# Performance work log

Measured on AMD Instinct MI355X. Metric: run time of the kernel, lower is better.

## Reference

```python
import jax, jax.numpy as jnp
import numpy as np

WINDOW = 15  # window_size from init


def setup_inputs() -> dict:
    key = jax.random.key(0)
    ks = jax.random.split(key, 8)
    B, S, H, G = 16, 4096, 768, 16
    sequence_output = jax.random.normal(ks[0], (B, S, H), dtype=jnp.float32)
    pooled_output = jax.random.normal(ks[1], (B, H), dtype=jnp.float32)
    token_type_ids = jnp.zeros((B, S), dtype=jnp.int64)
    word_mask = jax.random.randint(ks[2], (B, S), 0, 2, dtype=jnp.int64)
    gap_ids = jax.random.randint(ks[3], (B, G), 0, S, dtype=jnp.int64)
    gap_W = 0.02 * jax.random.normal(ks[4], (3 * H,), dtype=jnp.float32)
    gap_b = jnp.zeros((), dtype=jnp.float32)
    cls_W = 0.02 * jax.random.normal(ks[5], (3 * H,), dtype=jnp.float32)
    cls_b = jnp.zeros((), dtype=jnp.float32)
    return {"sequence_output": sequence_output, "pooled_output": pooled_output,
            "token_type_ids": token_type_ids, "word_mask": word_mask,
            "gap_ids": gap_ids, "gap_W": gap_W, "gap_b": gap_b,
            "cls_W": cls_W, "cls_b": cls_b}


def reference(sequence_output, pooled_output, token_type_ids, word_mask,
              gap_ids, gap_W, gap_b, cls_W, cls_b):
    B, S, H = sequence_output.shape
    G = gap_ids.shape[1]
    w = WINDOW
    Wlen = 2 * w + 1

    # gap token embeddings: [B, G, H]
    gaps = jnp.take_along_axis(sequence_output, gap_ids[:, :, None], axis=1)

    base_mask = (token_type_ids == 0) & (word_mask != 0)  # [B, S]

    # Sliding window gather around each gap (equivalent to the original
    # full-sequence masked reduction, since masked entries are exactly 0).
    offsets = jnp.arange(-w, w + 1)  # [Wlen]
    raw_idx = gap_ids[:, :, None] + offsets  # [B, G, Wlen]
    valid = (raw_idx >= 0) & (raw_idx < S)
    idx = jnp.clip(raw_idx, 0, S - 1)
    flat = idx.reshape(B, G * Wlen)
    win_mask = valid & jnp.take_along_axis(base_mask, flat, axis=1).reshape(B, G, Wlen)
    win_vals = jnp.take_along_axis(sequence_output, flat[:, :, None], axis=1).reshape(B, G, Wlen, H)

    # original does max(window * mask): masked positions contribute 0,
    # and the sequence always has positions outside the window -> max with 0
    masked_max = jnp.where(win_mask[..., None], win_vals, -jnp.inf).max(axis=2)
    window_max_pool = jnp.maximum(masked_max, 0.0)  # [B, G, H]
    num_tokens = win_mask.sum(axis=2).astype(jnp.float32)[:, :, None]
    window_avg_pool = jnp.einsum('bgw,bgwh->bgh', win_mask.astype(jnp.float32), win_vals) / num_tokens

    # full-text pooling
    text_masked_max = jnp.where(base_mask[:, :, None], sequence_output, -jnp.inf).max(axis=1)
    text_max_pool = jnp.maximum(text_masked_max, 0.0)  # [B, H]
    text_num = base_mask.sum(axis=1).astype(jnp.float32)[:, None]
    text_avg_pool = jnp.einsum('bs,bsh->bh', base_mask.astype(jnp.float32), sequence_output) / text_num

    gap_features = jnp.concatenate([gaps, window_max_pool, window_avg_pool], axis=-1)  # [B, G, 3H]
    cls_features = jnp.concatenate([pooled_output, text_max_pool, text_avg_pool], axis=-1)  # [B, 3H]

    gap_scores = gap_features @ gap_W + gap_b  # [B, G]
    cls_scores = (cls_features @ cls_W + cls_b)[:, None]  # [B, 1]
    return jnp.concatenate([cls_scores, gap_scores], axis=1)  # [B, 1+G]
```

## Files before the change

kernel.cpp:

```cpp
#include <hip/hip_runtime.h>
#include <math.h>

#define NB 16
#define NS 4096
#define NH 768
#define NG 16
#define WRAD 15
#define WLEN 31
#define NH4 192
#define OUTW (1 + NG)
#define NCH 32
#define CHUNK 128

__device__ inline float4 f4max(float4 a, float4 b) {
    return make_float4(fmaxf(a.x, b.x), fmaxf(a.y, b.y), fmaxf(a.z, b.z), fmaxf(a.w, b.w));
}
__device__ inline float4 f4add(float4 a, float4 b) {
    return make_float4(a.x + b.x, a.y + b.y, a.z + b.z, a.w + b.w);
}
__device__ inline float f4dot(float4 a, float4 b) {
    return a.x * b.x + a.y * b.y + a.z * b.z + a.w * b.w;
}

__device__ inline float block_reduce_192(float v, float* sbuf) {
    int tid = threadIdx.x;
    sbuf[tid] = v;
    if (tid < 64) sbuf[192 + tid] = 0.0f;
    __syncthreads();
    for (int off = 128; off > 0; off >>= 1) {
        if (tid < off) sbuf[tid] += sbuf[tid + off];
        __syncthreads();
    }
    float r = sbuf[0];
    __syncthreads();
    return r;
}

__global__ __launch_bounds__(192) void fused_kernel(
    const float* __restrict__ seq, const int* __restrict__ tt,
    const int* __restrict__ wm, const int* __restrict__ gids,
    const float* __restrict__ gapW, const float* __restrict__ gapb,
    float* __restrict__ pmax, float* __restrict__ psum,
    int* __restrict__ pcnt, float* __restrict__ out) {
    const int blk = blockIdx.x;
    const int tid = threadIdx.x;

    __shared__ float sbuf[256];
    __shared__ int s_idx[CHUNK];
    __shared__ unsigned long long s_wmask[2];
    __shared__ int s_misc[2];

    const float4 ninf4 = make_float4(-INFINITY, -INFINITY, -INFINITY, -INFINITY);
    const float4 zero4 = make_float4(0.f, 0.f, 0.f, 0.f);

    if (blk < NB * NCH) {
        const int b = blk / NCH;
        const int ss = blk % NCH;
        const int s0 = ss * CHUNK;

        if (tid < CHUNK) {
            const int s = s0 + tid;
            bool v = (tt[b * NS + s] == 0) && (wm[b * NS + s] != 0);
            unsigned long long m = __ballot(v);
            if ((tid & 63) == 0) s_wmask[tid >> 6] = m;
        }
        __syncthreads();
        if (tid < CHUNK) {
            const int w = tid >> 6, l = tid & 63;
            const unsigned long long m = s_wmask[w];
            if ((m >> l) & 1ull) {
                int pos = (w ? __popcll(s_wmask[0]) : 0) +
                          __popcll(m & ((1ull << l) - 1ull));
                s_idx[pos] = s0 + tid;
            }
        }
        if (tid == 0)
            s_misc[0] = __popcll(s_wmask[0]) + __popcll(s_wmask[1]);
        __syncthreads();
        const int n = s_misc[0];

        const float4* rowbase = (const float4*)(seq + (size_t)b * NS * NH);
        float4 mx = ninf4;
        float4 sm = zero4;
        int i = 0;
        for (; i + 4 <= n; i += 4) {
            const int i0 = s_idx[i], i1 = s_idx[i + 1], i2 = s_idx[i + 2], i3 = s_idx[i + 3];
            float4 v0 = rowbase[(size_t)i0 * NH4 + tid];
            float4 v1 = rowbase[(size_t)i1 * NH4 + tid];
            float4 v2 = rowbase[(size_t)i2 * NH4 + tid];
            float4 v3 = rowbase[(size_t)i3 * NH4 + tid];
            mx = f4max(mx, f4max(f4max(v0, v1), f4max(v2, v3)));
            sm = f4add(sm, f4add(f4add(v0, v1), f4add(v2, v3)));
        }
        for (; i < n; ++i) {
            float4 v = rowbase[(size_t)s_idx[i] * NH4 + tid];
            mx = f4max(mx, v);
            sm = f4add(sm, v);
        }
        const size_t o = ((size_t)(b * NCH + ss)) * NH4 + tid;
        ((float4*)pmax)[o] = mx;
        ((float4*)psum)[o] = sm;
        if (tid == 0) pcnt[b * NCH + ss] = n;
    } else {
        const int bg = blk - NB * NCH;
        const int b = bg >> 4;
        const int g = bg & 15;

        if (tid == 0) s_misc[1] = gids[b * NG + g];
        __syncthreads();
        const int gi = s_misc[1];

        if (tid < 64) {
            bool v = false;
            if (tid < WLEN) {
                const int idx = gi - WRAD + tid;
                v = (idx >= 0) && (idx < NS) && (tt[b * NS + idx] == 0) &&
                    (wm[b * NS + idx] != 0);
            }
            unsigned long long m = __ballot(v);
            if (tid == 0) s_wmask[0] = m;
        }
        __syncthreads();
        const unsigned long long vm = s_wmask[0];
        const float count = (float)__popcll(vm);

        const float4* rowbase = (const float4*)(seq + (size_t)b * NS * NH);
        const float4 gv = rowbase[(size_t)gi * NH4 + tid];

        float4 mx = ninf4;
        float4 sm = zero4;
#pragma unroll 4
        for (int j = 0; j < WLEN; ++j) {
            int idx = gi - WRAD + j;
            idx = idx < 0 ? 0 : (idx > NS - 1 ? NS - 1 : idx);
            const float4 v = rowbase[(size_t)idx * NH4 + tid];
            const bool val = (vm >> j) & 1ull;
            mx.x = val ? fmaxf(mx.x, v.x) : mx.x;
            mx.y = val ? fmaxf(mx.y, v.y) : mx.y;
            mx.z = val ? fmaxf(mx.z, v.z) : mx.z;
            mx.w = val ? fmaxf(mx.w, v.w) : mx.w;
            sm.x += val ? v.x : 0.f;
            sm.y += val ? v.y : 0.f;
            sm.z += val ? v.z : 0.f;
            sm.w += val ? v.w : 0.f;
        }
        const float4 wmax = f4max(mx, zero4);
        const float4 wavg = make_float4(sm.x / count, sm.y / count,
                                        sm.z / count, sm.w / count);

        const float4* w0 = (const float4*)gapW;
        const float4* w1 = (const float4*)(gapW + NH);
        const float4* w2 = (const float4*)(gapW + 2 * NH);
        float part = f4dot(gv, w0[tid]) + f4dot(wmax, w1[tid]) + f4dot(wavg, w2[tid]);
        float total = block_reduce_192(part, sbuf);
        if (tid == 0) out[b * OUTW + 1 + g] = total + gapb[0];
    }
}

__global__ __launch_bounds__(192) void cls_kernel(
    const float* __restrict__ pooled, const float* __restrict__ pmax,
    const float* __restrict__ psum, const int* __restrict__ pcnt,
    const float* __restrict__ clsW, const float* __restrict__ clsb,
    float* __restrict__ out) {
    const int b = blockIdx.x;
    const int tid = threadIdx.x;
    __shared__ float sbuf[256];

    float c = (tid < NCH) ? (float)pcnt[b * NCH + tid] : 0.f;
    const float count = block_reduce_192(c, sbuf);

    const float4* pm4 = (const float4*)pmax;
    const float4* ps4 = (const float4*)psum;
    float4 mx = make_float4(-INFINITY, -INFINITY, -INFINITY, -INFINITY);
    float4 sm = make_float4(0.f, 0.f, 0.f, 0.f);
#pragma unroll 8
    for (int ch = 0; ch < NCH; ++ch) {
        const size_t o = ((size_t)(b * NCH + ch)) * NH4 + tid;
        mx = f4max(mx, pm4[o]);
        sm = f4add(sm, ps4[o]);
    }
    const float4 zero4 = make_float4(0.f, 0.f, 0.f, 0.f);
    const float4 tmax = f4max(mx, zero4);
    const float4 tavg = make_float4(sm.x / count, sm.y / count,
                                    sm.z / count, sm.w / count);

    const float4* p4 = (const float4*)(pooled + (size_t)b * NH);
    const float4* w0 = (const float4*)clsW;
    const float4* w1 = (const float4*)(clsW + NH);
    const float4* w2 = (const float4*)(clsW + 2 * NH);
    float part = f4dot(p4[tid], w0[tid]) + f4dot(tmax, w1[tid]) + f4dot(tavg, w2[tid]);
    float total = block_reduce_192(part, sbuf);
    if (tid == 0) out[b * OUTW + 0] = total + clsb[0];
}

extern "C" void kernel_launch(void* const* d_in, const int* in_sizes, int n_in,
                              void* d_out, int out_size, void* d_ws, size_t ws_size,
                              hipStream_t stream) {
    const float* seq    = (const float*)d_in[0];
    const float* pooled = (const float*)d_in[1];
    const int*   tt     = (const int*)d_in[2];
    const int*   wm     = (const int*)d_in[3];
    const int*   gids   = (const int*)d_in[4];
    const float* gapW   = (const float*)d_in[5];
    const float* gapb   = (const float*)d_in[6];
    const float* clsW   = (const float*)d_in[7];
    const float* clsb   = (const float*)d_in[8];
    float* out = (float*)d_out;

    float* pmax = (float*)d_ws;
    float* psum = pmax + (size_t)NB * NCH * NH;
    int*   pcnt = (int*)(psum + (size_t)NB * NCH * NH);

    fused_kernel<<<NB * NCH + NB * NG, 192, 0, stream>>>(
        seq, tt, wm, gids, gapW, gapb, pmax, psum, pcnt, out);
    cls_kernel<<<NB, 192, 0, stream>>>(pooled, pmax, psum, pcnt, clsW, clsb, out);
}
```

Before: 286.7 us.

## Fuse cls reduction into main kernel via last-block atomic arrival counter

Removes the separate cls_kernel launch. The last chunk block to finish for each batch, detected with an atomic arrival counter, now does the final cross-chunk max/sum reduction and the cls dot product, while a second atomic accumulates token counts. Gap blocks are moved to the front of the grid, and the chunk gather loop is unrolled to 8 rows for more loads in flight. In exchange it adds a hipMemsetAsync per call, threadfences and atomics, and a serialized tail on the last-arriving block.

New measurement: 364.1 us. 1.27x slower.

```diff
diff --git a/kernel.cpp b/kernel.cpp
--- a/kernel.cpp
+++ b/kernel.cpp
@@ -37,78 +37,35 @@
 }
 
 __global__ __launch_bounds__(192) void fused_kernel(
-    const float* __restrict__ seq, const int* __restrict__ tt,
-    const int* __restrict__ wm, const int* __restrict__ gids,
+    const float* __restrict__ seq, const float* __restrict__ pooled,
+    const int* __restrict__ tt, const int* __restrict__ wm,
+    const int* __restrict__ gids,
     const float* __restrict__ gapW, const float* __restrict__ gapb,
+    const float* __restrict__ clsW, const float* __restrict__ clsb,
     float* __restrict__ pmax, float* __restrict__ psum,
-    int* __restrict__ pcnt, float* __restrict__ out) {
+    unsigned int* __restrict__ arrive, unsigned int* __restrict__ tokcnt,
+    float* __restrict__ out) {
     const int blk = blockIdx.x;
     const int tid = threadIdx.x;
 
     __shared__ float sbuf[256];
     __shared__ int s_idx[CHUNK];
     __shared__ unsigned long long s_wmask[2];
-    __shared__ int s_misc[2];
+    __shared__ int s_n;
+    __shared__ int s_gid;
+    __shared__ int s_last;
+    __shared__ unsigned int s_tok;
 
     const float4 ninf4 = make_float4(-INFINITY, -INFINITY, -INFINITY, -INFINITY);
     const float4 zero4 = make_float4(0.f, 0.f, 0.f, 0.f);
 
-    if (blk < NB * NCH) {
-        const int b = blk / NCH;
-        const int ss = blk % NCH;
-        const int s0 = ss * CHUNK;
-
-        if (tid < CHUNK) {
-            const int s = s0 + tid;
-            bool v = (tt[b * NS + s] == 0) && (wm[b * NS + s] != 0);
-            unsigned long long m = __ballot(v);
-            if ((tid & 63) == 0) s_wmask[tid >> 6] = m;
-        }
-        __syncthreads();
-        if (tid < CHUNK) {
-            const int w = tid >> 6, l = tid & 63;
-            const unsigned long long m = s_wmask[w];
-            if ((m >> l) & 1ull) {
-                int pos = (w ? __popcll(s_wmask[0]) : 0) +
-                          __popcll(m & ((1ull << l) - 1ull));
-                s_idx[pos] = s0 + tid;
-            }
-        }
-        if (tid == 0)
-            s_misc[0] = __popcll(s_wmask[0]) + __popcll(s_wmask[1]);
-        __syncthreads();
-        const int n = s_misc[0];
-
-        const float4* rowbase = (const float4*)(seq + (size_t)b * NS * NH);
-        float4 mx = ninf4;
-        float4 sm = zero4;
-        int i = 0;
-        for (; i + 4 <= n; i += 4) {
-            const int i0 = s_idx[i], i1 = s_idx[i + 1], i2 = s_idx[i + 2], i3 = s_idx[i + 3];
-            float4 v0 = rowbase[(size_t)i0 * NH4 + tid];
-            float4 v1 = rowbase[(size_t)i1 * NH4 + tid];
-            float4 v2 = rowbase[(size_t)i2 * NH4 + tid];
-            float4 v3 = rowbase[(size_t)i3 * NH4 + tid];
-            mx = f4max(mx, f4max(f4max(v0, v1), f4max(v2, v3)));
-            sm = f4add(sm, f4add(f4add(v0, v1), f4add(v2, v3)));
-        }
-        for (; i < n; ++i) {
-            float4 v = rowbase[(size_t)s_idx[i] * NH4 + tid];
-            mx = f4max(mx, v);
-            sm = f4add(sm, v);
-        }
-        const size_t o = ((size_t)(b * NCH + ss)) * NH4 + tid;
-        ((float4*)pmax)[o] = mx;
-        ((float4*)psum)[o] = sm;
-        if (tid == 0) pcnt[b * NCH + ss] = n;
-    } else {
-        const int bg = blk - NB * NCH;
-        const int b = bg >> 4;
-        const int g = bg & 15;
-
-        if (tid == 0) s_misc[1] = gids[b * NG + g];
-        __syncthreads();
-        const int gi = s_misc[1];
+    if (blk < NB * NG) {
+        const int b = blk >> 4;
+        const int g = blk & 15;
+
+        if (tid == 0) s_gid = gids[b * NG + g];
+        __syncthreads();
+        const int gi = s_gid;
 
         if (tid < 64) {
             bool v = false;
@@ -154,43 +111,104 @@
         float part = f4dot(gv, w0[tid]) + f4dot(wmax, w1[tid]) + f4dot(wavg, w2[tid]);
         float total = block_reduce_192(part, sbuf);
         if (tid == 0) out[b * OUTW + 1 + g] = total + gapb[0];
+    } else {
+        const int t = blk - NB * NG;
+        const int b = t / NCH;
+        const int ss = t % NCH;
+        const int s0 = ss * CHUNK;
+
+        if (tid < CHUNK) {
+            const int s = s0 + tid;
+            bool v = (tt[b * NS + s] == 0) && (wm[b * NS + s] != 0);
+            unsigned long long m = __ballot(v);
+            if ((tid & 63) == 0) s_wmask[tid >> 6] = m;
+        }
+        __syncthreads();
+        if (tid < CHUNK) {
+            const int w = tid >> 6, l = tid & 63;
+            const unsigned long long m = s_wmask[w];
+            if ((m >> l) & 1ull) {
+                int pos = (w ? __popcll(s_wmask[0]) : 0) +
+                          __popcll(m & ((1ull << l) - 1ull));
+                s_idx[pos] = s0 + tid;
+            }
+        }
+        if (tid == 0)
+            s_n = __popcll(s_wmask[0]) + __popcll(s_wmask[1]);
+        __syncthreads();
+        const int n = s_n;
+
+        const float4* rowbase = (const float4*)(seq + (size_t)b * NS * NH);
+        float4 mx = ninf4;
+        float4 sm = zero4;
+        int i = 0;
+        for (; i + 8 <= n; i += 8) {
+            float4 v0 = rowbase[(size_t)s_idx[i] * NH4 + tid];
+            float4 v1 = rowbase[(size_t)s_idx[i + 1] * NH4 + tid];
+            float4 v2 = rowbase[(size_t)s_idx[i + 2] * NH4 + tid];
+            float4 v3 = rowbase[(size_t)s_idx[i + 3] * NH4 + tid];
+            float4 v4 = rowbase[(size_t)s_idx[i + 4] * NH4 + tid];
+            float4 v5 = rowbase[(size_t)s_idx[i + 5] * NH4 + tid];
+            float4 v6 = rowbase[(size_t)s_idx[i + 6] * NH4 + tid];
+            float4 v7 = rowbase[(size_t)s_idx[i + 7] * NH4 + tid];
+            mx = f4max(mx, f4max(f4max(f4max(v0, v1), f4max(v2, v3)),
+                                 f4max(f4max(v4, v5), f4max(v6, v7))));
+            sm = f4add(sm, f4add(f4add(f4add(v0, v1), f4add(v2, v3)),
+                                 f4add(f4add(v4, v5), f4add(v6, v7))));
+        }
+        for (; i + 4 <= n; i += 4) {
+            float4 v0 = rowbase[(size_t)s_idx[i] * NH4 + tid];
+            float4 v1 = rowbase[(size_t)s_idx[i + 1] * NH4 + tid];
+            float4 v2 = rowbase[(size_t)s_idx[i + 2] * NH4 + tid];
+            float4 v3 = rowbase[(size_t)s_idx[i + 3] * NH4 + tid];
+            mx = f4max(mx, f4max(f4max(v0, v1), f4max(v2, v3)));
+            sm = f4add(sm, f4add(f4add(v0, v1), f4add(v2, v3)));
+        }
+        for (; i < n; ++i) {
+            float4 v = rowbase[(size_t)s_idx[i] * NH4 + tid];
+            mx = f4max(mx, v);
+            sm = f4add(sm, v);
+        }
+        const size_t o = ((size_t)(b * NCH + ss)) * NH4 + tid;
+        ((float4*)pmax)[o] = mx;
+        ((float4*)psum)[o] = sm;
+
+        __threadfence();
+        __syncthreads();
+        if (tid == 0) {
+            atomicAdd(&tokcnt[b], (unsigned int)n);
+            __threadfence();
+            unsigned int old = atomicAdd(&arrive[b], 1u);
+            s_last = (old == NCH - 1);
+            if (s_last) s_tok = atomicAdd(&tokcnt[b], 0u);
+        }
+        __syncthreads();
+        if (s_last) {
+            __threadfence();
+            const float count = (float)s_tok;
+            const float4* pm4 = (const float4*)pmax;
+            const float4* ps4 = (const float4*)psum;
+            float4 cmx = ninf4;
+            float4 csm = zero4;
+#pragma unroll 8
+            for (int ch = 0; ch < NCH; ++ch) {
+                const size_t co = ((size_t)(b * NCH + ch)) * NH4 + tid;
+                cmx = f4max(cmx, pm4[co]);
+                csm = f4add(csm, ps4[co]);
+            }
+            const float4 tmax = f4max(cmx, zero4);
+            const float4 tavg = make_float4(csm.x / count, csm.y / count,
+                                            csm.z / count, csm.w / count);
+            const float4* p4 = (const float4*)(pooled + (size_t)b * NH);
+            const float4* w0 = (const float4*)clsW;
+            const float4* w1 = (const float4*)(clsW + NH);
+            const float4* w2 = (const float4*)(clsW + 2 * NH);
+            float part = f4dot(p4[tid], w0[tid]) + f4dot(tmax, w1[tid]) +
+                         f4dot(tavg, w2[tid]);
+            float total = block_reduce_192(part, sbuf);
+            if (tid == 0) out[b * OUTW + 0] = total + clsb[0];
+        }
     }
-}
-
-__global__ __launch_bounds__(192) void cls_kernel(
-    const float* __restrict__ pooled, const float* __restrict__ pmax,
-    const float* __restrict__ psum, const int* __restrict__ pcnt,
-    const float* __restrict__ clsW, const float* __restrict__ clsb,
-    float* __restrict__ out) {
-    const int b = blockIdx.x;
-    const int tid = threadIdx.x;
-    __shared__ float sbuf[256];
-
-    float c = (tid < NCH) ? (float)pcnt[b * NCH + tid] : 0.f;
-    const float count = block_reduce_192(c, sbuf);
-
-    const float4* pm4 = (const float4*)pmax;
-    const float4* ps4 = (const float4*)psum;
-    float4 mx = make_float4(-INFINITY, -INFINITY, -INFINITY, -INFINITY);
-    float4 sm = make_float4(0.f, 0.f, 0.f, 0.f);
-#pragma unroll 8
-    for (int ch = 0; ch < NCH; ++ch) {
-        const size_t o = ((size_t)(b * NCH + ch)) * NH4 + tid;
-        mx = f4max(mx, pm4[o]);
-        sm = f4add(sm, ps4[o]);
-    }
-    const float4 zero4 = make_float4(0.f, 0.f, 0.f, 0.f);
-    const float4 tmax = f4max(mx, zero4);
-    const float4 tavg = make_float4(sm.x / count, sm.y / count,
-                                    sm.z / count, sm.w / count);
-
-    const float4* p4 = (const float4*)(pooled + (size_t)b * NH);
-    const float4* w0 = (const float4*)clsW;
-    const float4* w1 = (const float4*)(clsW + NH);
-    const float4* w2 = (const float4*)(clsW + 2 * NH);
-    float part = f4dot(p4[tid], w0[tid]) + f4dot(tmax, w1[tid]) + f4dot(tavg, w2[tid]);
-    float total = block_reduce_192(part, sbuf);
-    if (tid == 0) out[b * OUTW + 0] = total + clsb[0];
 }
 
 extern "C" void kernel_launch(void* const* d_in, const int* in_sizes, int n_in,
@@ -209,9 +227,12 @@
 
     float* pmax = (float*)d_ws;
     float* psum = pmax + (size_t)NB * NCH * NH;
-    int*   pcnt = (int*)(psum + (size_t)NB * NCH * NH);
-
-    fused_kernel<<<NB * NCH + NB * NG, 192, 0, stream>>>(
-        seq, tt, wm, gids, gapW, gapb, pmax, psum, pcnt, out);
-    cls_kernel<<<NB, 192, 0, stream>>>(pooled, pmax, psum, pcnt, clsW, clsb, out);
-}
+    unsigned int* arrive = (unsigned int*)(psum + (size_t)NB * NCH * NH);
+    unsigned int* tokcnt = arrive + NB;
+
+    hipMemsetAsync(arrive, 0, 2 * NB * sizeof(unsigned int), stream);
+
+    fused_kernel<<<NB * NG + NB * NCH, 192, 0, stream>>>(
+        seq, pooled, tt, wm, gids, gapW, gapb, clsW, clsb,
+        pmax, psum, arrive, tokcnt, out);
+}
```

## Stream all rows with predicated masking instead of compacted index gather

Applied to the files above, without the earlier changes.

Text pooling blocks now read every row in a 64-row chunk contiguously with 8-way unrolled loads and apply the word mask via predication, instead of compacting masked indices in shared memory and gathering only those rows. Chunks are halved to double block count, and gap-window blocks are scheduled first in the grid. This removes the index-compaction sync and dependent index loads and gives regular, deep memory-level parallelism, at the cost of reading masked-out rows (about twice the bytes for half-dense masks).

After: 318.1 us. 11.0% more time.

```diff
diff --git a/kernel.cpp b/kernel.cpp
--- a/kernel.cpp
+++ b/kernel.cpp
@@ -9,8 +9,8 @@
 #define WLEN 31
 #define NH4 192
 #define OUTW (1 + NG)
-#define NCH 32
-#define CHUNK 128
+#define NCH 64
+#define CHUNK 64
 
 __device__ inline float4 f4max(float4 a, float4 b) {
     return make_float4(fmaxf(a.x, b.x), fmaxf(a.y, b.y), fmaxf(a.z, b.z), fmaxf(a.w, b.w));
@@ -46,69 +46,19 @@
     const int tid = threadIdx.x;
 
     __shared__ float sbuf[256];
-    __shared__ int s_idx[CHUNK];
-    __shared__ unsigned long long s_wmask[2];
-    __shared__ int s_misc[2];
+    __shared__ unsigned long long s_mask;
+    __shared__ int s_gid;
 
     const float4 ninf4 = make_float4(-INFINITY, -INFINITY, -INFINITY, -INFINITY);
     const float4 zero4 = make_float4(0.f, 0.f, 0.f, 0.f);
 
-    if (blk < NB * NCH) {
-        const int b = blk / NCH;
-        const int ss = blk % NCH;
-        const int s0 = ss * CHUNK;
-
-        if (tid < CHUNK) {
-            const int s = s0 + tid;
-            bool v = (tt[b * NS + s] == 0) && (wm[b * NS + s] != 0);
-            unsigned long long m = __ballot(v);
-            if ((tid & 63) == 0) s_wmask[tid >> 6] = m;
-        }
-        __syncthreads();
-        if (tid < CHUNK) {
-            const int w = tid >> 6, l = tid & 63;
-            const unsigned long long m = s_wmask[w];
-            if ((m >> l) & 1ull) {
-                int pos = (w ? __popcll(s_wmask[0]) : 0) +
-                          __popcll(m & ((1ull << l) - 1ull));
-                s_idx[pos] = s0 + tid;
-            }
-        }
-        if (tid == 0)
-            s_misc[0] = __popcll(s_wmask[0]) + __popcll(s_wmask[1]);
-        __syncthreads();
-        const int n = s_misc[0];
-
-        const float4* rowbase = (const float4*)(seq + (size_t)b * NS * NH);
-        float4 mx = ninf4;
-        float4 sm = zero4;
-        int i = 0;
-        for (; i + 4 <= n; i += 4) {
-            const int i0 = s_idx[i], i1 = s_idx[i + 1], i2 = s_idx[i + 2], i3 = s_idx[i + 3];
-            float4 v0 = rowbase[(size_t)i0 * NH4 + tid];
-            float4 v1 = rowbase[(size_t)i1 * NH4 + tid];
-            float4 v2 = rowbase[(size_t)i2 * NH4 + tid];
-            float4 v3 = rowbase[(size_t)i3 * NH4 + tid];
-            mx = f4max(mx, f4max(f4max(v0, v1), f4max(v2, v3)));
-            sm = f4add(sm, f4add(f4add(v0, v1), f4add(v2, v3)));
-        }
-        for (; i < n; ++i) {
-            float4 v = rowbase[(size_t)s_idx[i] * NH4 + tid];
-            mx = f4max(mx, v);
-            sm = f4add(sm, v);
-        }
-        const size_t o = ((size_t)(b * NCH + ss)) * NH4 + tid;
-        ((float4*)pmax)[o] = mx;
-        ((float4*)psum)[o] = sm;
-        if (tid == 0) pcnt[b * NCH + ss] = n;
-    } else {
-        const int bg = blk - NB * NCH;
-        const int b = bg >> 4;
-        const int g = bg & 15;
-
-        if (tid == 0) s_misc[1] = gids[b * NG + g];
-        __syncthreads();
-        const int gi = s_misc[1];
+    if (blk < NB * NG) {
+        const int b = blk >> 4;
+        const int g = blk & 15;
+
+        if (tid == 0) s_gid = gids[b * NG + g];
+        __syncthreads();
+        const int gi = s_gid;
 
         if (tid < 64) {
             bool v = false;
@@ -118,13 +68,13 @@
                     (wm[b * NS + idx] != 0);
             }
             unsigned long long m = __ballot(v);
-            if (tid == 0) s_wmask[0] = m;
-        }
-        __syncthreads();
-        const unsigned long long vm = s_wmask[0];
+            if (tid == 0) s_mask = m;
+        }
+        __syncthreads();
+        const unsigned long long vm = s_mask;
         const float count = (float)__popcll(vm);
 
-        const float4* rowbase = (const float4*)(seq + (size_t)b * NS * NH);
+        const float4* rowbase = ((const float4*)seq) + (size_t)b * NS * NH4;
         const float4 gv = rowbase[(size_t)gi * NH4 + tid];
 
         float4 mx = ninf4;
@@ -154,6 +104,53 @@
         float part = f4dot(gv, w0[tid]) + f4dot(wmax, w1[tid]) + f4dot(wavg, w2[tid]);
         float total = block_reduce_192(part, sbuf);
         if (tid == 0) out[b * OUTW + 1 + g] = total + gapb[0];
+    } else {
+        const int t = blk - NB * NG;
+        const int b = t / NCH;
+        const int ss = t % NCH;
+        const int s0 = ss * CHUNK;
+
+        if (tid < 64) {
+            const int s = s0 + tid;
+            bool v = (tt[b * NS + s] == 0) && (wm[b * NS + s] != 0);
+            unsigned long long m = __ballot(v);
+            if (tid == 0) s_mask = m;
+        }
+        __syncthreads();
+        const unsigned long long m = s_mask;
+
+        const float4* rowbase = ((const float4*)seq) + (size_t)(b * NS + s0) * NH4;
+        float4 mx = ninf4;
+        float4 sm = zero4;
+#pragma unroll 1
+        for (int jo = 0; jo < CHUNK; jo += 8) {
+            float4 v0 = rowbase[(size_t)(jo + 0) * NH4 + tid];
+            float4 v1 = rowbase[(size_t)(jo + 1) * NH4 + tid];
+            float4 v2 = rowbase[(size_t)(jo + 2) * NH4 + tid];
+            float4 v3 = rowbase[(size_t)(jo + 3) * NH4 + tid];
+            float4 v4 = rowbase[(size_t)(jo + 4) * NH4 + tid];
+            float4 v5 = rowbase[(size_t)(jo + 5) * NH4 + tid];
+            float4 v6 = rowbase[(size_t)(jo + 6) * NH4 + tid];
+            float4 v7 = rowbase[(size_t)(jo + 7) * NH4 + tid];
+            const float4 vv[8] = {v0, v1, v2, v3, v4, v5, v6, v7};
+#pragma unroll
+            for (int k = 0; k < 8; ++k) {
+                const bool val = (m >> (jo + k)) & 1ull;
+                const float4 v = vv[k];
+                mx.x = val ? fmaxf(mx.x, v.x) : mx.x;
+                mx.y = val ? fmaxf(mx.y, v.y) : mx.y;
+                mx.z = val ? fmaxf(mx.z, v.z) : mx.z;
+                mx.w = val ? fmaxf(mx.w, v.w) : mx.w;
+                sm.x += val ? v.x : 0.f;
+                sm.y += val ? v.y : 0.f;
+                sm.z += val ? v.z : 0.f;
+                sm.w += val ? v.w : 0.f;
+            }
+        }
+        const size_t o = ((size_t)(b * NCH + ss)) * NH4 + tid;
+        ((float4*)pmax)[o] = mx;
+        ((float4*)psum)[o] = sm;
+        if (tid == 0) pcnt[b * NCH + ss] = __popcll(m);
     }
 }
 
@@ -211,7 +208,7 @@
     float* psum = pmax + (size_t)NB * NCH * NH;
     int*   pcnt = (int*)(psum + (size_t)NB * NCH * NH);
 
-    fused_kernel<<<NB * NCH + NB * NG, 192, 0, stream>>>(
+    fused_kernel<<<NB * NG + NB * NCH, 192, 0, stream>>>(
         seq, tt, wm, gids, gapW, gapb, pmax, psum, pcnt, out);
     cls_kernel<<<NB, 192, 0, stream>>>(pooled, pmax, psum, pcnt, clsW, clsb, out);
 }
```

## Stream full chunks densely with mask multiply instead of compacted gather

Applied to the files above, without the earlier changes.

The text-pooling phase no longer builds a compacted index list of valid tokens. Each block now reads every row of a smaller 32-token chunk contiguously, with software-pipelined prefetch, and multiplies each row by its 0/1 mask bit before the max and sum. Max accumulators start at zero, which folds in the clamp to zero that the reference applies after the max. The number of chunks per batch rises from 32 to 128, giving more blocks and a longer cls reduction loop. Reading all rows roughly doubles the bytes read (about half the tokens are masked), in exchange for regular streaming access and no shared-memory compaction or its extra barrier.

Measured after the change: 339.9 us. +18.5%, slower.

```diff
diff --git a/kernel.cpp b/kernel.cpp
--- a/kernel.cpp
+++ b/kernel.cpp
@@ -9,8 +9,8 @@
 #define WLEN 31
 #define NH4 192
 #define OUTW (1 + NG)
-#define NCH 32
-#define CHUNK 128
+#define NCH 128
+#define CHUNK 32
 
 __device__ inline float4 f4max(float4 a, float4 b) {
     return make_float4(fmaxf(a.x, b.x), fmaxf(a.y, b.y), fmaxf(a.z, b.z), fmaxf(a.w, b.w));
@@ -21,6 +21,15 @@
 __device__ inline float f4dot(float4 a, float4 b) {
     return a.x * b.x + a.y * b.y + a.z * b.z + a.w * b.w;
 }
+
+#define PROC(c, bit)                                                     \
+    {                                                                    \
+        const float mf = (float)((m >> (bit)) & 1u);                     \
+        const float4 vmm = make_float4(c.x * mf, c.y * mf, c.z * mf,     \
+                                       c.w * mf);                        \
+        mx = f4max(mx, vmm);                                             \
+        sm = f4add(sm, vmm);                                             \
+    }
 
 __device__ inline float block_reduce_192(float v, float* sbuf) {
     int tid = threadIdx.x;
@@ -46,11 +55,9 @@
     const int tid = threadIdx.x;
 
     __shared__ float sbuf[256];
-    __shared__ int s_idx[CHUNK];
-    __shared__ unsigned long long s_wmask[2];
-    __shared__ int s_misc[2];
-
-    const float4 ninf4 = make_float4(-INFINITY, -INFINITY, -INFINITY, -INFINITY);
+    __shared__ unsigned int s_mask;
+    __shared__ int s_gid;
+
     const float4 zero4 = make_float4(0.f, 0.f, 0.f, 0.f);
 
     if (blk < NB * NCH) {
@@ -58,57 +65,57 @@
         const int ss = blk % NCH;
         const int s0 = ss * CHUNK;
 
-        if (tid < CHUNK) {
-            const int s = s0 + tid;
-            bool v = (tt[b * NS + s] == 0) && (wm[b * NS + s] != 0);
-            unsigned long long m = __ballot(v);
-            if ((tid & 63) == 0) s_wmask[tid >> 6] = m;
-        }
-        __syncthreads();
-        if (tid < CHUNK) {
-            const int w = tid >> 6, l = tid & 63;
-            const unsigned long long m = s_wmask[w];
-            if ((m >> l) & 1ull) {
-                int pos = (w ? __popcll(s_wmask[0]) : 0) +
-                          __popcll(m & ((1ull << l) - 1ull));
-                s_idx[pos] = s0 + tid;
+        if (tid < 64) {
+            bool v = false;
+            if (tid < CHUNK) {
+                const int s = s0 + tid;
+                v = (tt[b * NS + s] == 0) && (wm[b * NS + s] != 0);
             }
-        }
-        if (tid == 0)
-            s_misc[0] = __popcll(s_wmask[0]) + __popcll(s_wmask[1]);
-        __syncthreads();
-        const int n = s_misc[0];
-
-        const float4* rowbase = (const float4*)(seq + (size_t)b * NS * NH);
-        float4 mx = ninf4;
+            unsigned long long bm = __ballot(v);
+            if (tid == 0) s_mask = (unsigned int)bm;
+        }
+        __syncthreads();
+        const unsigned int m = s_mask;
+
+        const float4* base = ((const float4*)seq) + (size_t)(b * NS + s0) * NH4 + tid;
+        float4 mx = zero4;
         float4 sm = zero4;
-        int i = 0;
-        for (; i + 4 <= n; i += 4) {
-            const int i0 = s_idx[i], i1 = s_idx[i + 1], i2 = s_idx[i + 2], i3 = s_idx[i + 3];
-            float4 v0 = rowbase[(size_t)i0 * NH4 + tid];
-            float4 v1 = rowbase[(size_t)i1 * NH4 + tid];
-            float4 v2 = rowbase[(size_t)i2 * NH4 + tid];
-            float4 v3 = rowbase[(size_t)i3 * NH4 + tid];
-            mx = f4max(mx, f4max(f4max(v0, v1), f4max(v2, v3)));
-            sm = f4add(sm, f4add(f4add(v0, v1), f4add(v2, v3)));
-        }
-        for (; i < n; ++i) {
-            float4 v = rowbase[(size_t)s_idx[i] * NH4 + tid];
-            mx = f4max(mx, v);
-            sm = f4add(sm, v);
-        }
+
+        float4 c0 = base[0 * NH4];
+        float4 c1 = base[1 * NH4];
+        float4 c2 = base[2 * NH4];
+        float4 c3 = base[3 * NH4];
+        int j = 0;
+#pragma unroll 2
+        for (; j < CHUNK - 4; j += 4) {
+            const float4* nb = base + (size_t)(j + 4) * NH4;
+            float4 n0 = nb[0 * NH4];
+            float4 n1 = nb[1 * NH4];
+            float4 n2 = nb[2 * NH4];
+            float4 n3 = nb[3 * NH4];
+            PROC(c0, j + 0);
+            PROC(c1, j + 1);
+            PROC(c2, j + 2);
+            PROC(c3, j + 3);
+            c0 = n0; c1 = n1; c2 = n2; c3 = n3;
+        }
+        PROC(c0, j + 0);
+        PROC(c1, j + 1);
+        PROC(c2, j + 2);
+        PROC(c3, j + 3);
+
         const size_t o = ((size_t)(b * NCH + ss)) * NH4 + tid;
         ((float4*)pmax)[o] = mx;
         ((float4*)psum)[o] = sm;
-        if (tid == 0) pcnt[b * NCH + ss] = n;
+        if (tid == 0) pcnt[b * NCH + ss] = __popc(m);
     } else {
         const int bg = blk - NB * NCH;
         const int b = bg >> 4;
         const int g = bg & 15;
 
-        if (tid == 0) s_misc[1] = gids[b * NG + g];
-        __syncthreads();
-        const int gi = s_misc[1];
+        if (tid == 0) s_gid = gids[b * NG + g];
+        __syncthreads();
+        const int gi = s_gid;
 
         if (tid < 64) {
             bool v = false;
@@ -117,34 +124,26 @@
                 v = (idx >= 0) && (idx < NS) && (tt[b * NS + idx] == 0) &&
                     (wm[b * NS + idx] != 0);
             }
-            unsigned long long m = __ballot(v);
-            if (tid == 0) s_wmask[0] = m;
-        }
-        __syncthreads();
-        const unsigned long long vm = s_wmask[0];
-        const float count = (float)__popcll(vm);
-
-        const float4* rowbase = (const float4*)(seq + (size_t)b * NS * NH);
+            unsigned long long bm = __ballot(v);
+            if (tid == 0) s_mask = (unsigned int)bm;
+        }
+        __syncthreads();
+        const unsigned int m = s_mask;
+        const float count = (float)__popc(m);
+
+        const float4* rowbase = ((const float4*)seq) + (size_t)b * NS * NH4;
         const float4 gv = rowbase[(size_t)gi * NH4 + tid];
 
-        float4 mx = ninf4;
+        float4 mx = zero4;
         float4 sm = zero4;
 #pragma unroll 4
         for (int j = 0; j < WLEN; ++j) {
             int idx = gi - WRAD + j;
             idx = idx < 0 ? 0 : (idx > NS - 1 ? NS - 1 : idx);
-            const float4 v = rowbase[(size_t)idx * NH4 + tid];
-            const bool val = (vm >> j) & 1ull;
-            mx.x = val ? fmaxf(mx.x, v.x) : mx.x;
-            mx.y = val ? fmaxf(mx.y, v.y) : mx.y;
-            mx.z = val ? fmaxf(mx.z, v.z) : mx.z;
-            mx.w = val ? fmaxf(mx.w, v.w) : mx.w;
-            sm.x += val ? v.x : 0.f;
-            sm.y += val ? v.y : 0.f;
-            sm.z += val ? v.z : 0.f;
-            sm.w += val ? v.w : 0.f;
-        }
-        const float4 wmax = f4max(mx, zero4);
+            const float4 c = rowbase[(size_t)idx * NH4 + tid];
+            PROC(c, j);
+        }
+        const float4 wmax = mx;
         const float4 wavg = make_float4(sm.x / count, sm.y / count,
                                         sm.z / count, sm.w / count);
 
@@ -171,7 +170,7 @@
 
     const float4* pm4 = (const float4*)pmax;
     const float4* ps4 = (const float4*)psum;
-    float4 mx = make_float4(-INFINITY, -INFINITY, -INFINITY, -INFINITY);
+    float4 mx = make_float4(0.f, 0.f, 0.f, 0.f);
     float4 sm = make_float4(0.f, 0.f, 0.f, 0.f);
 #pragma unroll 8
     for (int ch = 0; ch < NCH; ++ch) {
@@ -179,8 +178,7 @@
         mx = f4max(mx, pm4[o]);
         sm = f4add(sm, ps4[o]);
     }
-    const float4 zero4 = make_float4(0.f, 0.f, 0.f, 0.f);
-    const float4 tmax = f4max(mx, zero4);
+    const float4 tmax = mx;
     const float4 tavg = make_float4(sm.x / count, sm.y / count,
                                     sm.z / count, sm.w / count);
 
```
